# Kernel tuning notes

Measured on AMD Instinct MI355X. Metric: run time of the kernel, lower is better.

Reference implementation:

```python
import jax, jax.numpy as jnp
import numpy as np

D_MODEL = 1024
NUM_HEADS = 16
DEPTH = D_MODEL // NUM_HEADS  # 64
BATCH, SEQ = 4, 2048


def setup_inputs() -> dict:
    key = jax.random.key(0)
    ks = jax.random.split(key, 9)
    s = 1.0 / np.sqrt(D_MODEL)
    x = jax.random.normal(ks[0], (BATCH, SEQ, D_MODEL), dtype=jnp.float32)
    # Per-head Dense weights stacked on a leading head axis [H, d_model, depth]
    Wq = jax.random.normal(ks[1], (NUM_HEADS, D_MODEL, DEPTH), dtype=jnp.float32) * s
    Wk = jax.random.normal(ks[2], (NUM_HEADS, D_MODEL, DEPTH), dtype=jnp.float32) * s
    Wv = jax.random.normal(ks[3], (NUM_HEADS, D_MODEL, DEPTH), dtype=jnp.float32) * s
    bq = jnp.zeros((NUM_HEADS, DEPTH), dtype=jnp.float32)
    bk = jnp.zeros((NUM_HEADS, DEPTH), dtype=jnp.float32)
    bv = jnp.zeros((NUM_HEADS, DEPTH), dtype=jnp.float32)
    Wo = jax.random.normal(ks[4], (D_MODEL, D_MODEL), dtype=jnp.float32) * s
    bo = jnp.zeros((D_MODEL,), dtype=jnp.float32)
    return {"x": x, "Wq": Wq, "bq": bq, "Wk": Wk, "bk": bk,
            "Wv": Wv, "bv": bv, "Wo": Wo, "bo": bo}


def reference(x, Wq, bq, Wk, bk, Wv, bv, Wo, bo):
    # Batched equivalent of the per-head loop: project, attend, concat heads.
    q = jnp.einsum('bsd,hde->bhse', x, Wq) + bq[:, None, :]  # [B,H,S,depth]
    k = jnp.einsum('bsd,hde->bhse', x, Wk) + bk[:, None, :]
    v = jnp.einsum('bsd,hde->bhse', x, Wv) + bv[:, None, :]
    scale = 1.0 / jnp.sqrt(jnp.asarray(DEPTH, dtype=x.dtype))
    scores = jnp.einsum('bhse,bhte->bhst', q, k) * scale      # [B,H,S,S]
    weights = jax.nn.softmax(scores, axis=-1)
    heads = jnp.einsum('bhst,bhte->bhse', weights, v)         # [B,H,S,depth]
    # concat head outputs along last axis in head order (tf.concat axis=-1)
    multi = jnp.transpose(heads, (0, 2, 1, 3)).reshape(x.shape[0], x.shape[1], D_MODEL)
    return multi @ Wo + bo
```

## Files before the change

kernel.cpp:

```cpp
#include <hip/hip_runtime.h>
#include <hip/hip_bf16.h>

#define BATCH 4
#define SEQ   2048
#define DM    1024
#define NH    16
#define DEPTH 64
#define ROWS  (BATCH*SEQ)
#define NQKV  (3*DM)
#define BH    (BATCH*NH)

typedef __attribute__((ext_vector_type(8))) short bf16x8;
typedef __attribute__((ext_vector_type(4))) float f32x4;
typedef __attribute__((ext_vector_type(16))) float f32x16;
typedef unsigned short u16;
typedef unsigned int   u32;

__device__ __forceinline__ u16 f2bf(float f) {
    union { float f; unsigned u; } v; v.f = f;
    unsigned r = v.u + 0x7fff + ((v.u >> 16) & 1);
    return (u16)(r >> 16);
}

__device__ __forceinline__ u32 pk2bf(float a, float b) {
#if __has_builtin(__builtin_amdgcn_cvt_pk_bf16_f32)
    typedef __attribute__((ext_vector_type(2))) __bf16 v2bf;
    union { v2bf v; u32 u; } u_;
    u_.v = __builtin_amdgcn_cvt_pk_bf16_f32(a, b);
    return u_.u;
#else
    return (u32)f2bf(a) | ((u32)f2bf(b) << 16);
#endif
}

__device__ __forceinline__ void plswap(u32 a, u32 b, u32& x, u32& y) {
#if __has_builtin(__builtin_amdgcn_permlane32_swap)
    typedef __attribute__((ext_vector_type(2))) int i32x2;
    i32x2 r = __builtin_amdgcn_permlane32_swap((int)a, (int)b, false, false);
    x = (u32)r.x; y = (u32)r.y;
#else
    u32 as = (u32)__shfl_xor((int)a, 32);
    u32 bs = (u32)__shfl_xor((int)b, 32);
    int h = (threadIdx.x >> 5) & 1;
    x = h ? bs : a;
    y = h ? b : as;
#endif
}

__device__ __forceinline__ void g2l16(void* lds, const void* g) {
    __builtin_amdgcn_global_load_lds((const __attribute__((address_space(1))) void*)g,
                                     (__attribute__((address_space(3))) void*)lds, 16, 0, 0);
}

__device__ __forceinline__ bf16x8 frag8(const u16* tile, int row, int gl) {
    return *(const bf16x8*)(tile + row * 64 + ((gl ^ (row & 7)) * 8));
}

__device__ __forceinline__ f32x16 mfma32(bf16x8 a, bf16x8 b, f32x16 c) {
    return __builtin_amdgcn_mfma_f32_32x32x16_bf16(a, b, c, 0, 0, 0);
}

__global__ __launch_bounds__(256) void k_prep(const float* __restrict__ x,
                                              const float* __restrict__ Wq, const float* __restrict__ Wk,
                                              const float* __restrict__ Wv, const float* __restrict__ Wo,
                                              u16* __restrict__ xb, u16* __restrict__ BT, u16* __restrict__ WoT) {
    __shared__ u16 T[64][65];
    int tid = threadIdx.x;
    int bx = blockIdx.x;
    if (bx < 2048) {
        int i = bx * 4096 + tid * 4;
        for (int l = 0; l < 4; ++l) {
            float4 v = *(const float4*)(x + i + l * 1024);
            ushort4 o; o.x = f2bf(v.x); o.y = f2bf(v.y); o.z = f2bf(v.z); o.w = f2bf(v.w);
            *(ushort4*)(xb + i + l * 1024) = o;
        }
        return;
    }
    if (bx < 2816) {
        int q = bx - 2048;
        int kt = q & 15, mh = q >> 4, m = mh >> 4, h = mh & 15;
        const float* W = (m == 0) ? Wq : (m == 1) ? Wk : Wv;
        const float* src = W + ((size_t)h * 1024 + kt * 64) * 64;
        int e = tid & 63, r0 = tid >> 6;
        for (int i = 0; i < 16; ++i) { int r = i * 4 + r0; T[r][e] = f2bf(src[r * 64 + e]); }
        __syncthreads();
        int kk = tid & 63, e0 = tid >> 6;
        u16* dst = BT + ((size_t)m * 1024 + h * 64) * 1024 + kt * 64;
        for (int i = 0; i < 16; ++i) { int ee = i * 4 + e0; dst[ee * 1024 + kk] = T[kk][ee]; }
        return;
    }
    {
        int q = bx - 2816;
        int kt = q & 15, nt = q >> 4;
        const float* src = Wo + (size_t)kt * 64 * 1024 + nt * 64;
        int c = tid & 63, r0 = tid >> 6;
        for (int i = 0; i < 16; ++i) { int r = i * 4 + r0; T[r][c] = f2bf(src[r * 1024 + c]); }
        __syncthreads();
        int kk = tid & 63, e0 = tid >> 6;
        u16* dst = WoT + (size_t)nt * 64 * 1024 + kt * 64;
        for (int i = 0; i < 16; ++i) { int ee = i * 4 + e0; dst[ee * 1024 + kk] = T[kk][ee]; }
    }
}

__global__ __launch_bounds__(256, 2) void k_gemm_qkv(const u16* __restrict__ xb, const u16* __restrict__ Wt,
                                                     const float* __restrict__ bq, const float* __restrict__ bk,
                                                     const float* __restrict__ bv,
                                                     u16* __restrict__ Q, u16* __restrict__ K, u16* __restrict__ VT) {
    __shared__ u16 Al[2][128 * 64];
    __shared__ u16 Bl[2][128 * 64];
    int tid = threadIdx.x;
    int wave = tid >> 6, lane = tid & 63, l31 = lane & 31, h2 = lane >> 5;
    int wr = wave >> 1, wc = wave & 1;

    int b = blockIdx.x;
    int wg = (b & 7) * 192 + (b >> 3);

    bool isvt = (wg >= 1024);
    int row0, col0;
    const u16 *Am, *Bm;
    if (!isvt) {
        row0 = (wg >> 4) * 128; col0 = (wg & 15) * 128;
        Am = xb + (size_t)row0 * 1024;
        Bm = Wt + (size_t)col0 * 1024;
    } else {
        int b2 = wg - 1024;
        row0 = (b2 >> 6) * 128; col0 = (b2 & 63) * 128;
        Am = Wt + (size_t)(2048 + row0) * 1024;
        Bm = xb + (size_t)col0 * 1024;
    }

    f32x16 acc[2][2] = {};

#pragma unroll
    for (int l = 0; l < 4; ++l) {
        int idx = tid + l * 256, r = idx >> 3, gs = ((idx & 7) ^ (r & 7)) * 8;
        g2l16(&Al[0][idx * 8], Am + r * 1024 + gs);
        g2l16(&Bl[0][idx * 8], Bm + r * 1024 + gs);
    }
    __syncthreads();

    for (int t = 0; t < 16; ++t) {
        int cur = t & 1;
        if (t < 15) {
            int k0 = (t + 1) * 64;
#pragma unroll
            for (int l = 0; l < 4; ++l) {
                int idx = tid + l * 256, r = idx >> 3, gs = ((idx & 7) ^ (r & 7)) * 8;
                g2l16(&Al[cur ^ 1][idx * 8], Am + r * 1024 + k0 + gs);
                g2l16(&Bl[cur ^ 1][idx * 8], Bm + r * 1024 + k0 + gs);
            }
        }
        __builtin_amdgcn_s_setprio(1);
#pragma unroll
        for (int kk = 0; kk < 4; ++kk) {
            bf16x8 a[2], bb[2];
#pragma unroll
            for (int mi = 0; mi < 2; ++mi) a[mi] = frag8(Al[cur], wr * 64 + mi * 32 + l31, 2 * kk + h2);
#pragma unroll
            for (int ni = 0; ni < 2; ++ni) bb[ni] = frag8(Bl[cur], wc * 64 + ni * 32 + l31, 2 * kk + h2);
#pragma unroll
            for (int mi = 0; mi < 2; ++mi)
#pragma unroll
                for (int ni = 0; ni < 2; ++ni)
                    acc[mi][ni] = mfma32(a[mi], bb[ni], acc[mi][ni]);
        }
        __builtin_amdgcn_s_setprio(0);
        __syncthreads();
    }

    if (!isvt) {
        const float QSCALE = 0.125f * 1.4426950408889634f;
        int m = (col0 >= 1024);
        const float* bias = m ? bk : bq;
        u16* dst0 = m ? K : Q;
#pragma unroll
        for (int ni = 0; ni < 2; ++ni) {
            int c = col0 + wc * 64 + ni * 32 + l31;
            int h = (c >> 6) & 15, e = c & 63;
            float bval = bias[h * 64 + e];
#pragma unroll
            for (int mi = 0; mi < 2; ++mi)
#pragma unroll
                for (int reg = 0; reg < 16; ++reg) {
                    int rowg = row0 + wr * 64 + mi * 32 + (reg & 3) + 8 * (reg >> 2) + 4 * h2;
                    int b_ = rowg >> 11, s = rowg & 2047;
                    int bh = b_ * 16 + h;
                    float v = acc[mi][ni][reg] + bval;
                    if (!m) v *= QSCALE;
                    dst0[((size_t)bh * 2048 + s) * 64 + e] = f2bf(v);
                }
        }
    } else {
#pragma unroll
        for (int ni = 0; ni < 2; ++ni) {
            int c = col0 + wc * 64 + ni * 32 + l31;
            int b_ = c >> 11, s = c & 2047;
#pragma unroll
            for (int mi = 0; mi < 2; ++mi)
#pragma unroll
                for (int reg = 0; reg < 16; ++reg) {
                    int ii = row0 + wr * 64 + mi * 32 + (reg & 3) + 8 * (reg >> 2) + 4 * h2;
                    float v = acc[mi][ni][reg] + bv[ii];
                    VT[((size_t)b_ * 1024 + ii) * 2048 + s] = f2bf(v);
                }
        }
    }
}

__global__ __launch_bounds__(256, 4) void k_attn(const u16* __restrict__ Q, const u16* __restrict__ K,
                                                 const u16* __restrict__ VT, u16* __restrict__ A2) {
    __shared__ u16 Kl[2][64 * 64];
    __shared__ u16 Vl[2][64 * 64];
    __shared__ float linv[128];
    int tid = threadIdx.x;
    int wave = tid >> 6, lane = tid & 63, l31 = lane & 31, h = lane >> 5;
    int bh = blockIdx.y;
    int m0 = blockIdx.x * 128;
    const u16* Qb = Q + (size_t)bh * 2048 * 64;
    const u16* Kb = K + (size_t)bh * 2048 * 64;
    const u16* Vb = VT + (size_t)bh * 64 * 2048;

    const u16* kp[2]; const u16* vp[2]; int dsti[2];
    for (int l = 0; l < 2; ++l) {
        int idx = tid + l * 256, r = idx >> 3, gs = ((idx & 7) ^ (r & 7)) * 8;
        dsti[l] = idx * 8;
        kp[l] = Kb + r * 64 + gs;
        vp[l] = Vb + r * 2048 + gs;
    }

    bf16x8 qb[4];
    {
        const u16* q0 = Qb + (size_t)(m0 + wave * 32 + l31) * 64 + h * 8;
#pragma unroll
        for (int s = 0; s < 4; ++s) qb[s] = *(const bf16x8*)(q0 + s * 16);
    }

    for (int l = 0; l < 2; ++l) { g2l16(&Kl[0][dsti[l]], kp[l]); g2l16(&Vl[0][dsti[l]], vp[l]); }
    __syncthreads();

    f32x16 oacc[2] = {};
    float lsum = 0.f;

    for (int t = 0; t < 32; ++t) {
        int cur = t & 1;
        if (t < 31) {
            for (int l = 0; l < 2; ++l) {
                g2l16(&Kl[cur ^ 1][dsti[l]], kp[l] + (t + 1) * 4096);
                g2l16(&Vl[cur ^ 1][dsti[l]], vp[l] + (t + 1) * 64);
            }
        }

        f32x16 sc[2] = {};
        __builtin_amdgcn_s_setprio(1);
#pragma unroll
        for (int s = 0; s < 4; ++s) {
            bf16x8 kf0 = frag8(Kl[cur], l31,      2 * s + h);
            bf16x8 kf1 = frag8(Kl[cur], 32 + l31, 2 * s + h);
            sc[0] = mfma32(kf0, qb[s], sc[0]);
            sc[1] = mfma32(kf1, qb[s], sc[1]);
        }
        __builtin_amdgcn_s_setprio(0);

        bf16x8 pa[4];
        float sq = 0.f;
#pragma unroll
        for (int kt = 0; kt < 2; ++kt)
#pragma unroll
            for (int gp = 0; gp < 2; ++gp) {
                float e00 = __builtin_amdgcn_exp2f(sc[kt][(2 * gp) * 4 + 0]);
                float e01 = __builtin_amdgcn_exp2f(sc[kt][(2 * gp) * 4 + 1]);
                float e02 = __builtin_amdgcn_exp2f(sc[kt][(2 * gp) * 4 + 2]);
                float e03 = __builtin_amdgcn_exp2f(sc[kt][(2 * gp) * 4 + 3]);
                float e10 = __builtin_amdgcn_exp2f(sc[kt][(2 * gp + 1) * 4 + 0]);
                float e11 = __builtin_amdgcn_exp2f(sc[kt][(2 * gp + 1) * 4 + 1]);
                float e12 = __builtin_amdgcn_exp2f(sc[kt][(2 * gp + 1) * 4 + 2]);
                float e13 = __builtin_amdgcn_exp2f(sc[kt][(2 * gp + 1) * 4 + 3]);
                sq += ((e00 + e01) + (e02 + e03)) + ((e10 + e11) + (e12 + e13));
                u32 ue = pk2bf(e00, e01), ve = pk2bf(e02, e03);
                u32 uo = pk2bf(e10, e11), vo = pk2bf(e12, e13);
                u32 w0, w1, w2, w3;
                plswap(ue, uo, w0, w2);
                plswap(ve, vo, w1, w3);
                union { bf16x8 v; u32 w[4]; } pu;
                pu.w[0] = w0; pu.w[1] = w1; pu.w[2] = w2; pu.w[3] = w3;
                pa[2 * kt + gp] = pu.v;
            }
        lsum += sq;

        __builtin_amdgcn_s_setprio(1);
#pragma unroll
        for (int s = 0; s < 4; ++s) {
            bf16x8 bv0 = frag8(Vl[cur], l31,      2 * s + h);
            bf16x8 bv1 = frag8(Vl[cur], 32 + l31, 2 * s + h);
            oacc[0] = mfma32(pa[s], bv0, oacc[0]);
            oacc[1] = mfma32(pa[s], bv1, oacc[1]);
        }
        __builtin_amdgcn_s_setprio(0);

        __syncthreads();
    }

    {
        float l2 = lsum + __shfl_xor(lsum, 32);
        linv[wave * 32 + l31] = 1.0f / l2;
    }
    int b_ = bh >> 4, hh = bh & 15;
    for (int g = 0; g < 4; ++g) {
        f32x4 iv = *(f32x4*)&linv[wave * 32 + 8 * g + 4 * h];
        for (int dt = 0; dt < 2; ++dt)
            for (int r = 0; r < 4; ++r) {
                int row = b_ * 2048 + m0 + wave * 32 + 8 * g + 4 * h + r;
                A2[row * 1024 + hh * 64 + dt * 32 + l31] = f2bf(oacc[dt][g * 4 + r] * iv[r]);
            }
    }
}

__global__ __launch_bounds__(256, 2) void k_gemm_out(const u16* __restrict__ A, const u16* __restrict__ BT,
                                                     const float* __restrict__ bo, float* __restrict__ out) {
    __shared__ u16 Al[2][128 * 64];
    __shared__ u16 Bl[2][128 * 64];
    int tid = threadIdx.x;
    int wave = tid >> 6, lane = tid & 63, l31 = lane & 31, h2 = lane >> 5;
    int wr = wave >> 1, wc = wave & 1;

    int b = blockIdx.x;
    int wg = (b & 7) * 64 + (b >> 3);
    int row0 = (wg >> 3) * 128, col0 = (wg & 7) * 128;

    const u16* Am = A  + (size_t)row0 * 1024;
    const u16* Bm = BT + (size_t)col0 * 1024;

    f32x16 acc[2][2] = {};

#pragma unroll
    for (int l = 0; l < 4; ++l) {
        int idx = tid + l * 256, r = idx >> 3, gs = ((idx & 7) ^ (r & 7)) * 8;
        g2l16(&Al[0][idx * 8], Am + r * 1024 + gs);
        g2l16(&Bl[0][idx * 8], Bm + r * 1024 + gs);
    }
    __syncthreads();

    for (int t = 0; t < 16; ++t) {
        int cur = t & 1;
        if (t < 15) {
            int k0 = (t + 1) * 64;
#pragma unroll
            for (int l = 0; l < 4; ++l) {
                int idx = tid + l * 256, r = idx >> 3, gs = ((idx & 7) ^ (r & 7)) * 8;
                g2l16(&Al[cur ^ 1][idx * 8], Am + r * 1024 + k0 + gs);
                g2l16(&Bl[cur ^ 1][idx * 8], Bm + r * 1024 + k0 + gs);
            }
        }
        __builtin_amdgcn_s_setprio(1);
#pragma unroll
        for (int kk = 0; kk < 4; ++kk) {
            bf16x8 a[2], bb[2];
#pragma unroll
            for (int mi = 0; mi < 2; ++mi) a[mi] = frag8(Al[cur], wr * 64 + mi * 32 + l31, 2 * kk + h2);
#pragma unroll
            for (int ni = 0; ni < 2; ++ni) bb[ni] = frag8(Bl[cur], wc * 64 + ni * 32 + l31, 2 * kk + h2);
#pragma unroll
            for (int mi = 0; mi < 2; ++mi)
#pragma unroll
                for (int ni = 0; ni < 2; ++ni)
                    acc[mi][ni] = mfma32(a[mi], bb[ni], acc[mi][ni]);
        }
        __builtin_amdgcn_s_setprio(0);
        __syncthreads();
    }

#pragma unroll
    for (int ni = 0; ni < 2; ++ni) {
        int c = col0 + wc * 64 + ni * 32 + l31;
        float bias = bo[c];
#pragma unroll
        for (int mi = 0; mi < 2; ++mi)
#pragma unroll
            for (int reg = 0; reg < 16; ++reg) {
                int rowg = row0 + wr * 64 + mi * 32 + (reg & 3) + 8 * (reg >> 2) + 4 * h2;
                out[(size_t)rowg * 1024 + c] = acc[mi][ni][reg] + bias;
            }
    }
}

extern "C" void kernel_launch(void* const* d_in, const int* in_sizes, int n_in,
                              void* d_out, int out_size, void* d_ws, size_t ws_size,
                              hipStream_t stream) {
    const float* x  = (const float*)d_in[0];
    const float* Wq = (const float*)d_in[1];
    const float* bq = (const float*)d_in[2];
    const float* Wk = (const float*)d_in[3];
    const float* bk = (const float*)d_in[4];
    const float* Wv = (const float*)d_in[5];
    const float* bv = (const float*)d_in[6];
    const float* Wo = (const float*)d_in[7];
    const float* bo = (const float*)d_in[8];
    float* out = (float*)d_out;

    char* ws = (char*)d_ws;
    u16* xb    = (u16*)ws; ws += (size_t)ROWS * DM * 2;
    u16* WqkvT = (u16*)ws; ws += (size_t)NQKV * DM * 2;
    u16* WoT   = (u16*)ws; ws += (size_t)DM * DM * 2;
    u16* Qb    = (u16*)ws; ws += (size_t)BH * SEQ * DEPTH * 2;
    u16* Kb    = (u16*)ws; ws += (size_t)BH * SEQ * DEPTH * 2;
    u16* VTb   = (u16*)ws; ws += (size_t)BH * SEQ * DEPTH * 2;
    u16* A2    = xb;
    (void)ws_size;

    k_prep     <<<dim3(3072),   dim3(256), 0, stream>>>(x, Wq, Wk, Wv, Wo, xb, WqkvT, WoT);
    k_gemm_qkv <<<dim3(1536),   dim3(256), 0, stream>>>(xb, WqkvT, bq, bk, bv, Qb, Kb, VTb);
    k_attn     <<<dim3(16, 64), dim3(256), 0, stream>>>(Qb, Kb, VTb, A2);
    k_gemm_out <<<dim3(512),    dim3(256), 0, stream>>>(A2, WoT, bo, out);
}
```

Baseline: 293.8 us.

## Prefetch two K-tiles ahead in GEMMs with partial vmcnt waits

Restructures the QKV-projection and output-projection GEMM main loops so two K-tiles are in flight at once. Each iteration waits only until the older tile's loads have landed (vmcnt(8)) instead of draining all loads at __syncthreads. The refill of the just-consumed buffer is issued after a barrier, and the last tile is peeled out of the loop. The aim is to hide global-to-LDS load latency behind MFMA work. The correctness of the raw waitcnt counts depends on g2l16 emitting exactly the assumed number of vector memory ops per stage.

```diff
diff --git a/kernel.cpp b/kernel.cpp
--- a/kernel.cpp
+++ b/kernel.cpp
@@ -131,42 +131,48 @@
 
     f32x16 acc[2][2] = {};
 
+    int sr[4], sgs[4], sdst[4];
 #pragma unroll
     for (int l = 0; l < 4; ++l) {
-        int idx = tid + l * 256, r = idx >> 3, gs = ((idx & 7) ^ (r & 7)) * 8;
-        g2l16(&Al[0][idx * 8], Am + r * 1024 + gs);
-        g2l16(&Bl[0][idx * 8], Bm + r * 1024 + gs);
-    }
-    __syncthreads();
-
-    for (int t = 0; t < 16; ++t) {
+        int idx = tid + l * 256;
+        sr[l] = idx >> 3; sgs[l] = ((idx & 7) ^ (sr[l] & 7)) * 8; sdst[l] = idx * 8;
+    }
+
+#define QKV_STAGE(bufi, k0) \
+    { _Pragma("unroll") for (int l = 0; l < 4; ++l) { \
+        g2l16(&Al[bufi][sdst[l]], Am + sr[l] * 1024 + (k0) + sgs[l]); \
+        g2l16(&Bl[bufi][sdst[l]], Bm + sr[l] * 1024 + (k0) + sgs[l]); } }
+
+#define QKV_COMPUTE(bufi) \
+    { _Pragma("unroll") for (int kk = 0; kk < 4; ++kk) { \
+        bf16x8 a_[2], bb_[2]; \
+        _Pragma("unroll") for (int mi = 0; mi < 2; ++mi) a_[mi] = frag8(Al[bufi], wr * 64 + mi * 32 + l31, 2 * kk + h2); \
+        _Pragma("unroll") for (int ni = 0; ni < 2; ++ni) bb_[ni] = frag8(Bl[bufi], wc * 64 + ni * 32 + l31, 2 * kk + h2); \
+        _Pragma("unroll") for (int mi = 0; mi < 2; ++mi) \
+        _Pragma("unroll") for (int ni = 0; ni < 2; ++ni) \
+            acc[mi][ni] = mfma32(a_[mi], bb_[ni], acc[mi][ni]); } }
+
+    QKV_STAGE(0, 0)
+    QKV_STAGE(1, 64)
+
+    for (int t = 0; t < 15; ++t) {
         int cur = t & 1;
-        if (t < 15) {
-            int k0 = (t + 1) * 64;
-#pragma unroll
-            for (int l = 0; l < 4; ++l) {
-                int idx = tid + l * 256, r = idx >> 3, gs = ((idx & 7) ^ (r & 7)) * 8;
-                g2l16(&Al[cur ^ 1][idx * 8], Am + r * 1024 + k0 + gs);
-                g2l16(&Bl[cur ^ 1][idx * 8], Bm + r * 1024 + k0 + gs);
-            }
-        }
+        asm volatile("s_waitcnt vmcnt(8)" ::: "memory");
+        __builtin_amdgcn_s_barrier();
+        asm volatile("" ::: "memory");
         __builtin_amdgcn_s_setprio(1);
-#pragma unroll
-        for (int kk = 0; kk < 4; ++kk) {
-            bf16x8 a[2], bb[2];
-#pragma unroll
-            for (int mi = 0; mi < 2; ++mi) a[mi] = frag8(Al[cur], wr * 64 + mi * 32 + l31, 2 * kk + h2);
-#pragma unroll
-            for (int ni = 0; ni < 2; ++ni) bb[ni] = frag8(Bl[cur], wc * 64 + ni * 32 + l31, 2 * kk + h2);
-#pragma unroll
-            for (int mi = 0; mi < 2; ++mi)
-#pragma unroll
-                for (int ni = 0; ni < 2; ++ni)
-                    acc[mi][ni] = mfma32(a[mi], bb[ni], acc[mi][ni]);
-        }
+        QKV_COMPUTE(cur)
         __builtin_amdgcn_s_setprio(0);
-        __syncthreads();
-    }
+        asm volatile("" ::: "memory");
+        __builtin_amdgcn_s_barrier();
+        if (t < 14) QKV_STAGE(cur, (t + 2) * 64)
+    }
+    asm volatile("s_waitcnt vmcnt(0)" ::: "memory");
+    __builtin_amdgcn_s_barrier();
+    asm volatile("" ::: "memory");
+    QKV_COMPUTE(1)
+#undef QKV_STAGE
+#undef QKV_COMPUTE
 
     if (!isvt) {
         const float QSCALE = 0.125f * 1.4426950408889634f;
@@ -332,42 +338,48 @@
 
     f32x16 acc[2][2] = {};
 
+    int sr[4], sgs[4], sdst[4];
 #pragma unroll
     for (int l = 0; l < 4; ++l) {
-        int idx = tid + l * 256, r = idx >> 3, gs = ((idx & 7) ^ (r & 7)) * 8;
-        g2l16(&Al[0][idx * 8], Am + r * 1024 + gs);
-        g2l16(&Bl[0][idx * 8], Bm + r * 1024 + gs);
-    }
-    __syncthreads();
-
-    for (int t = 0; t < 16; ++t) {
+        int idx = tid + l * 256;
+        sr[l] = idx >> 3; sgs[l] = ((idx & 7) ^ (sr[l] & 7)) * 8; sdst[l] = idx * 8;
+    }
+
+#define OUT_STAGE(bufi, k0) \
+    { _Pragma("unroll") for (int l = 0; l < 4; ++l) { \
+        g2l16(&Al[bufi][sdst[l]], Am + sr[l] * 1024 + (k0) + sgs[l]); \
+        g2l16(&Bl[bufi][sdst[l]], Bm + sr[l] * 1024 + (k0) + sgs[l]); } }
+
+#define OUT_COMPUTE(bufi) \
+    { _Pragma("unroll") for (int kk = 0; kk < 4; ++kk) { \
+        bf16x8 a_[2], bb_[2]; \
+        _Pragma("unroll") for (int mi = 0; mi < 2; ++mi) a_[mi] = frag8(Al[bufi], wr * 64 + mi * 32 + l31, 2 * kk + h2); \
+        _Pragma("unroll") for (int ni = 0; ni < 2; ++ni) bb_[ni] = frag8(Bl[bufi], wc * 64 + ni * 32 + l31, 2 * kk + h2); \
+        _Pragma("unroll") for (int mi = 0; mi < 2; ++mi) \
+        _Pragma("unroll") for (int ni = 0; ni < 2; ++ni) \
+            acc[mi][ni] = mfma32(a_[mi], bb_[ni], acc[mi][ni]); } }
+
+    OUT_STAGE(0, 0)
+    OUT_STAGE(1, 64)
+
+    for (int t = 0; t < 15; ++t) {
         int cur = t & 1;
-        if (t < 15) {
-            int k0 = (t + 1) * 64;
-#pragma unroll
-            for (int l = 0; l < 4; ++l) {
-                int idx = tid + l * 256, r = idx >> 3, gs = ((idx & 7) ^ (r & 7)) * 8;
-                g2l16(&Al[cur ^ 1][idx * 8], Am + r * 1024 + k0 + gs);
-                g2l16(&Bl[cur ^ 1][idx * 8], Bm + r * 1024 + k0 + gs);
-            }
-        }
+        asm volatile("s_waitcnt vmcnt(8)" ::: "memory");
+        __builtin_amdgcn_s_barrier();
+        asm volatile("" ::: "memory");
         __builtin_amdgcn_s_setprio(1);
-#pragma unroll
-        for (int kk = 0; kk < 4; ++kk) {
-            bf16x8 a[2], bb[2];
-#pragma unroll
-            for (int mi = 0; mi < 2; ++mi) a[mi] = frag8(Al[cur], wr * 64 + mi * 32 + l31, 2 * kk + h2);
-#pragma unroll
-            for (int ni = 0; ni < 2; ++ni) bb[ni] = frag8(Bl[cur], wc * 64 + ni * 32 + l31, 2 * kk + h2);
-#pragma unroll
-            for (int mi = 0; mi < 2; ++mi)
-#pragma unroll
-                for (int ni = 0; ni < 2; ++ni)
-                    acc[mi][ni] = mfma32(a[mi], bb[ni], acc[mi][ni]);
-        }
+        OUT_COMPUTE(cur)
         __builtin_amdgcn_s_setprio(0);
-        __syncthreads();
-    }
+        asm volatile("" ::: "memory");
+        __builtin_amdgcn_s_barrier();
+        if (t < 14) OUT_STAGE(cur, (t + 2) * 64)
+    }
+    asm volatile("s_waitcnt vmcnt(0)" ::: "memory");
+    __builtin_amdgcn_s_barrier();
+    asm volatile("" ::: "memory");
+    OUT_COMPUTE(1)
+#undef OUT_STAGE
+#undef OUT_COMPUTE
 
 #pragma unroll
     for (int ni = 0; ni < 2; ++ni) {
```

Result: slower. 301.0 us (+2.5%).
